# Kernel optimization log

Hardware: AMD Instinct MI355X
Metric: run time of the kernel (lower is better)

## Reference

```python
import jax, jax.numpy as jnp
import numpy as np

NUM_CLOTHES = 50000
FEAT_DIM = 256
BATCH = 1024
MOMENTUM = 0.0
SCALE = 16.0
EPSILON = 0.1


def setup_inputs() -> dict:
    key = jax.random.key(0)
    k1, k2, k3, k4 = jax.random.split(key, 4)
    inputs = jax.random.normal(k1, (BATCH, FEAT_DIM), dtype=jnp.float32)
    feature_memory = jax.random.normal(k2, (NUM_CLOTHES, FEAT_DIM), dtype=jnp.float32)
    targets = jax.random.randint(k3, (BATCH,), 0, NUM_CLOTHES, dtype=jnp.int64)
    # binary positive mask; guarantee the identity (own-clothes) column is positive
    positive_mask = (jax.random.uniform(k4, (BATCH, NUM_CLOTHES)) < 0.01).astype(jnp.float32)
    positive_mask = positive_mask.at[jnp.arange(BATCH), targets].set(1.0)
    return {"inputs": inputs, "feature_memory": feature_memory,
            "positive_mask": positive_mask, "targets": targets}


def _l2_normalize(x, axis=-1):
    # matches F.normalize(p=2): divide by max(||x||, 1e-12)
    n = jnp.sqrt(jnp.sum(x * x, axis=axis, keepdims=True))
    return x / jnp.maximum(n, 1e-12)


def reference(inputs, feature_memory, positive_mask, targets):
    B = inputs.shape[0]
    # ---- memory update: scatter-mean of detached features per clothes label ----
    feats = jax.lax.stop_gradient(inputs)
    sums = jax.ops.segment_sum(feats, targets, num_segments=NUM_CLOTHES)      # [C, D]
    counts = jax.ops.segment_sum(jnp.ones((B,), feats.dtype), targets,
                                 num_segments=NUM_CLOTHES)                     # [C]
    mean = sums / jnp.maximum(counts, 1.0)[:, None]
    present = (counts > 0)[:, None]
    memory = jnp.where(present,
                       MOMENTUM * feature_memory + (1.0 - MOMENTUM) * mean,
                       feature_memory)                                         # [C, D]
    memory = jax.lax.stop_gradient(memory)
    # ---- similarities against memory bank ----
    inputs_norm = _l2_normalize(inputs)
    memory_norm = _l2_normalize(memory)
    similarities = jnp.einsum('bd,cd->bc', inputs_norm, memory_norm) * SCALE   # [B, C]
    # ---- masked log-sum-exp loss ----
    negative_mask = 1.0 - positive_mask
    mask_identity = jax.nn.one_hot(targets, NUM_CLOTHES, dtype=similarities.dtype)
    exp_logits = jnp.exp(similarities)
    neg_sum = jnp.sum(exp_logits * negative_mask, axis=1, keepdims=True)       # [B, 1]
    log_prob = similarities - jnp.log(neg_sum + exp_logits)
    pos_count = jnp.sum(positive_mask, axis=1, keepdims=True)
    mask = (1.0 - EPSILON) * mask_identity + (EPSILON / pos_count) * positive_mask
    loss = jnp.mean(jnp.sum(-mask * log_prob, axis=1))
    return loss
```

## Files before the change

### kernel.cpp

```cpp
#include <hip/hip_runtime.h>
#include <hip/hip_bf16.h>
#include <stdint.h>

#define NCLOTHES 50000
#define CPAD     50048
#define NWORDS   782
#define NCB2     782
#define FDIM     256
#define NBATCH   1024
#define SCALEF   16.0f
#define EPSW     0.1f
#define SLOTS    8

typedef __attribute__((ext_vector_type(8))) short short8;
typedef __attribute__((ext_vector_type(4))) float f32x4;

__device__ __forceinline__ void gload_lds16(const void* gsrc, void* ldst) {
    __builtin_amdgcn_global_load_lds(
        (const __attribute__((address_space(1))) void*)gsrc,
        (__attribute__((address_space(3))) void*)ldst, 16, 0, 0);
}

__global__ __launch_bounds__(256)
void prep1_kernel(const float* __restrict__ in, const float* __restrict__ fm,
                  const float* __restrict__ pm,
                  __hip_bfloat16* __restrict__ A, __hip_bfloat16* __restrict__ Bm,
                  unsigned long long* __restrict__ maskw) {
    const int blk = blockIdx.x;
    const int t = threadIdx.x;

    if (blk < 1024) {
        int b = blk;
        float x = in[b * FDIM + t];
        float ss = x * x;
        #pragma unroll
        for (int o = 32; o > 0; o >>= 1) ss += __shfl_xor(ss, o);
        __shared__ float sh[4];
        if ((t & 63) == 0) sh[t >> 6] = ss;
        __syncthreads();
        float tot = sh[0] + sh[1] + sh[2] + sh[3];
        float r = SCALEF / fmaxf(sqrtf(tot), 1e-12f);
        A[b * FDIM + t] = __float2bfloat16(x * r);
    } else if (blk < 3072) {
        int p = blk - 1024;
        const int row = p >> 1;
        const int half = p & 1;
        const int wave = t >> 6;
        const int lane = t & 63;
        const float* prow = pm + (size_t)row * NCLOTHES;
        unsigned long long* wrow = maskw + (size_t)row * NWORDS;
        for (int chunk = half * 98 + wave; chunk < half * 98 + 98; chunk += 4) {
            int base = chunk * 256;
            int c0 = base + lane;
            float v0 = (c0 < NCLOTHES) ? prow[c0] : 0.f;
            float v1 = (c0 + 64 < NCLOTHES) ? prow[c0 + 64] : 0.f;
            float v2 = (c0 + 128 < NCLOTHES) ? prow[c0 + 128] : 0.f;
            float v3 = (c0 + 192 < NCLOTHES) ? prow[c0 + 192] : 0.f;
            unsigned long long b0 = __ballot(v0 >= 0.5f);
            unsigned long long b1 = __ballot(v1 >= 0.5f);
            unsigned long long b2 = __ballot(v2 >= 0.5f);
            unsigned long long b3 = __ballot(v3 >= 0.5f);
            if (lane < 4) {
                int wi = chunk * 4 + lane;
                unsigned long long w = (lane == 0) ? b0 : (lane == 1) ? b1 : (lane == 2) ? b2 : b3;
                if (wi < NWORDS) wrow[wi] = w;
            }
        }
    } else {
        const int nw = 2048 * 4;
        int w = ((blk - 3072) * 256 + t) >> 6;
        int lane = t & 63;
        for (int row = w; row < CPAD; row += nw) {
            __hip_bfloat16 h[4];
            if (row >= NCLOTHES) {
                h[0] = h[1] = h[2] = h[3] = __float2bfloat16(0.f);
            } else {
                f32x4 v = *(const f32x4*)(fm + (size_t)row * FDIM + lane * 4);
                float ss = v.x * v.x + v.y * v.y + v.z * v.z + v.w * v.w;
                #pragma unroll
                for (int o = 32; o > 0; o >>= 1) ss += __shfl_xor(ss, o);
                float r = 1.f / fmaxf(sqrtf(ss), 1e-12f);
                h[0] = __float2bfloat16(v.x * r);
                h[1] = __float2bfloat16(v.y * r);
                h[2] = __float2bfloat16(v.z * r);
                h[3] = __float2bfloat16(v.w * r);
            }
            *(ushort4*)(Bm + (size_t)row * FDIM + lane * 4) = *(const ushort4*)h;
        }
    }
}

__global__ void bnorm_present(const float* __restrict__ in, const int* __restrict__ tg,
                              __hip_bfloat16* __restrict__ Bm) {
    int b = blockIdx.x, t = threadIdx.x;
    __shared__ int stg[NBATCH];
    #pragma unroll
    for (int j = 0; j < 4; ++j) stg[t + j * 256] = tg[t + j * 256];
    __syncthreads();
    int c = stg[b];
    bool dup = false;
    #pragma unroll
    for (int j = 0; j < 4; ++j) {
        int i = t + j * 256;
        if (i < b && stg[i] == c) dup = true;
    }
    if (__syncthreads_or(dup)) return;
    __shared__ int mlist[64];
    __shared__ int mcount;
    if (t == 0) mcount = 0;
    __syncthreads();
    #pragma unroll
    for (int j = 0; j < 4; ++j) {
        int i = t + j * 256;
        if (stg[i] == c) { int p = atomicAdd(&mcount, 1); if (p < 64) mlist[p] = i; }
    }
    __syncthreads();
    int n = mcount;
    float v = 0.f;
    for (int i = 0; i < n; ++i) v += in[mlist[i] * FDIM + t];
    v /= (float)n;
    float ss = v * v;
    #pragma unroll
    for (int o = 32; o > 0; o >>= 1) ss += __shfl_xor(ss, o);
    __shared__ float sh[4];
    if ((t & 63) == 0) sh[t >> 6] = ss;
    __syncthreads();
    float tot = sh[0] + sh[1] + sh[2] + sh[3];
    float r = 1.0f / fmaxf(sqrtf(tot), 1e-12f);
    Bm[(size_t)c * FDIM + t] = __float2bfloat16(v * r);
}

#define BM 128
#define BN 128
#define BK 32
#define NKSTEP (FDIM / BK)

__global__ __launch_bounds__(256, 4)
void gemm_kernel(const __hip_bfloat16* __restrict__ A, const __hip_bfloat16* __restrict__ Bm,
                 const unsigned long long* __restrict__ maskw,
                 float* __restrict__ partial_ns,
                 float* __restrict__ sbuf)
{
    __shared__ alignas(16) __hip_bfloat16 As[2][BM * BK];
    __shared__ alignas(16) __hip_bfloat16 Bs[2][BM * BK];

    const int t = threadIdx.x;
    const int bx = blockIdx.x;
    const int bn0 = bx * BN;
    const int bm0 = blockIdx.y * BM;

    const int lane = t & 63;
    const int wave = t >> 6;
    const int wr = wave >> 1, wc = wave & 1;
    const int lrow = lane & 15, lq = lane >> 4;

    const int sr = t >> 2;
    const int sk = (t & 3) * 8;

    f32x4 acc[4][4];
    #pragma unroll
    for (int m = 0; m < 4; ++m)
        #pragma unroll
        for (int n = 0; n < 4; ++n) acc[m][n] = (f32x4)0.f;

    {
        const __hip_bfloat16* ag = A + (size_t)(bm0 + sr) * FDIM + sk;
        const __hip_bfloat16* bg = Bm + (size_t)(bn0 + sr) * FDIM + sk;
        gload_lds16(ag,             (void*)&As[0][t * 8]);
        gload_lds16(ag + 64 * FDIM, (void*)&As[0][2048 + t * 8]);
        gload_lds16(bg,             (void*)&Bs[0][t * 8]);
        gload_lds16(bg + 64 * FDIM, (void*)&Bs[0][2048 + t * 8]);
    }

    for (int ks = 0; ks < NKSTEP; ++ks) {
        __syncthreads();
        int cur = ks & 1;
        if (ks + 1 < NKSTEP) {
            int nxt = cur ^ 1;
            int k0 = (ks + 1) * BK;
            const __hip_bfloat16* ag = A + (size_t)(bm0 + sr) * FDIM + k0 + sk;
            const __hip_bfloat16* bg = Bm + (size_t)(bn0 + sr) * FDIM + k0 + sk;
            gload_lds16(ag,             (void*)&As[nxt][t * 8]);
            gload_lds16(ag + 64 * FDIM, (void*)&As[nxt][2048 + t * 8]);
            gload_lds16(bg,             (void*)&Bs[nxt][t * 8]);
            gload_lds16(bg + 64 * FDIM, (void*)&Bs[nxt][2048 + t * 8]);
        }
        short8 af[4], bf[4];
        #pragma unroll
        for (int m = 0; m < 4; ++m)
            af[m] = *(const short8*)&As[cur][(wr * 64 + m * 16 + lrow) * BK + lq * 8];
        #pragma unroll
        for (int n = 0; n < 4; ++n)
            bf[n] = *(const short8*)&Bs[cur][(wc * 64 + n * 16 + lrow) * BK + lq * 8];
        #pragma unroll
        for (int m = 0; m < 4; ++m)
            #pragma unroll
            for (int n = 0; n < 4; ++n)
                acc[m][n] = __builtin_amdgcn_mfma_f32_16x16x32_bf16(af[m], bf[n], acc[m][n], 0, 0, 0);
    }

    const int rowbase = bm0 + wr * 64;
    const int colbase = bn0 + wc * 64;
    const int cb2 = bx * 2 + wc;

    #pragma unroll
    for (int m = 0; m < 4; ++m) {
        #pragma unroll
        for (int r = 0; r < 4; ++r) {
            const int grow = rowbase + m * 16 + lq * 4 + r;
            const unsigned long long mw = maskw[(size_t)grow * NWORDS + cb2];
            float pneg = 0.f;
            #pragma unroll
            for (int n = 0; n < 4; ++n) {
                const int p = n * 16 + lrow;
                bool vld = (colbase + p) < NCLOTHES;
                bool pos = (mw >> p) & 1ull;
                pneg += (vld && !pos) ? __expf(acc[m][n][r]) : 0.f;
            }
            pneg += __shfl_xor(pneg, 1);
            pneg += __shfl_xor(pneg, 2);
            pneg += __shfl_xor(pneg, 4);
            pneg += __shfl_xor(pneg, 8);
            const size_t srow = (size_t)grow * NCB2 + cb2;
            #pragma unroll
            for (int n = 0; n < 4; ++n) {
                const int p = n * 16 + lrow;
                if ((mw >> p) & 1ull) {
                    int pre = __popcll(mw & ((1ull << p) - 1ull));
                    if (pre < SLOTS) sbuf[srow * SLOTS + pre] = acc[m][n][r];
                }
            }
            if (lrow == 0) partial_ns[(size_t)cb2 * NBATCH + grow] = pneg;
        }
    }
}

__global__ void nsum_kernel(const float* __restrict__ partial_ns, float* __restrict__ negsum) {
    int b = blockIdx.x * 256 + threadIdx.x;
    float s = 0.f;
    #pragma unroll 8
    for (int cb = 0; cb < NCB2; ++cb) s += partial_ns[(size_t)cb * NBATCH + b];
    negsum[b] = s;
}

__global__ void finish_kernel(const float* __restrict__ negsum,
                              const unsigned long long* __restrict__ maskw,
                              const float* __restrict__ sbuf,
                              const int* __restrict__ tg, float* __restrict__ loss_rows) {
    int b = blockIdx.x, t = threadIdx.x;
    int tgt = tg[b];
    const int cbt = tgt >> 6, bitp = tgt & 63;
    const float ns = negsum[b];

    const unsigned long long* mrow = maskw + (size_t)b * NWORDS;
    const float* srow = sbuf + (size_t)b * NCB2 * SLOTS;

    float slp = 0.f, idlp = 0.f;
    int np = 0;
    for (int cb = t; cb < NCB2; cb += 256) {
        unsigned long long mw = mrow[cb];
        if (mw) {
            int k = __popcll(mw);
            np += k;
            int kk = k < SLOTS ? k : SLOTS;
            const float* sp = srow + (size_t)cb * SLOTS;
            for (int i = 0; i < kk; ++i) {
                float s = sp[i];
                slp += s - __logf(ns + __expf(s));
            }
            if (cb == cbt) {
                int idslot = __popcll(mw & ((1ull << bitp) - 1ull));
                if (idslot < SLOTS) {
                    float s = sp[idslot];
                    idlp = s - __logf(ns + __expf(s));
                }
            }
        }
    }
    #pragma unroll
    for (int o = 32; o > 0; o >>= 1) {
        slp += __shfl_xor(slp, o);
        idlp += __shfl_xor(idlp, o);
        np += __shfl_xor(np, o);
    }
    __shared__ float sh1[4], sh2[4];
    __shared__ int shp[4];
    if ((t & 63) == 0) { sh1[t >> 6] = slp; sh2[t >> 6] = idlp; shp[t >> 6] = np; }
    __syncthreads();
    if (t == 0) {
        float s_all = sh1[0] + sh1[1] + sh1[2] + sh1[3];
        float i_all = sh2[0] + sh2[1] + sh2[2] + sh2[3];
        int np_all = shp[0] + shp[1] + shp[2] + shp[3];
        loss_rows[b] = -((1.0f - EPSW) * i_all + (EPSW / (float)np_all) * s_all);
    }
}

__global__ void reduce_kernel(const float* __restrict__ lr, float* __restrict__ out) {
    int t = threadIdx.x;
    float s = lr[t] + lr[t + 256] + lr[t + 512] + lr[t + 768];
    #pragma unroll
    for (int o = 32; o > 0; o >>= 1) s += __shfl_xor(s, o);
    __shared__ float sh[4];
    if ((t & 63) == 0) sh[t >> 6] = s;
    __syncthreads();
    if (t == 0) out[0] = (sh[0] + sh[1] + sh[2] + sh[3]) * (1.0f / NBATCH);
}

extern "C" void kernel_launch(void* const* d_in, const int* in_sizes, int n_in,
                              void* d_out, int out_size, void* d_ws, size_t ws_size,
                              hipStream_t stream) {
    const float* inputs  = (const float*)d_in[0];
    const float* fm      = (const float*)d_in[1];
    const float* pmask   = (const float*)d_in[2];
    const int*   targets = (const int*)d_in[3];
    float* out = (float*)d_out;

    char* ws = (char*)d_ws;
    size_t off = 0;
    __hip_bfloat16* A = (__hip_bfloat16*)(ws + off);  off += (size_t)NBATCH * FDIM * 2;
    __hip_bfloat16* Bm = (__hip_bfloat16*)(ws + off); off += (size_t)CPAD * FDIM * 2;
    off = (off + 255) & ~(size_t)255;
    unsigned long long* maskw = (unsigned long long*)(ws + off); off += (size_t)NBATCH * NWORDS * 8;
    float* partial_ns = (float*)(ws + off);        off += (size_t)NCB2 * NBATCH * 4;
    float* sbuf = (float*)(ws + off);              off += (size_t)NBATCH * NCB2 * SLOTS * 4;
    float* negsum = (float*)(ws + off);            off += 4096;
    float* loss_rows = (float*)(ws + off);         off += 4096;

    prep1_kernel<<<5120, 256, 0, stream>>>(inputs, fm, pmask, A, Bm, maskw);
    bnorm_present<<<NBATCH, 256, 0, stream>>>(inputs, targets, Bm);
    gemm_kernel<<<dim3(CPAD / BN, NBATCH / BM), 256, 0, stream>>>(A, Bm, maskw, partial_ns, sbuf);
    nsum_kernel<<<4, 256, 0, stream>>>(partial_ns, negsum);
    finish_kernel<<<NBATCH, 256, 0, stream>>>(negsum, maskw, sbuf, targets, loss_rows);
    reduce_kernel<<<1, 256, 0, stream>>>(loss_rows, out);
}
```

Before: 502.6 us.

## Keep 64-column memory tile resident in LDS and stream batch rows through

The GEMM now gives each block a 64-column slice of the normalized memory bank. That slice is loaded into LDS once, with XOR swizzling, and the block loops over all 1024 batch rows in 128-row chunks, double-buffering only the A tiles. Each memory-bank row is read from global memory once instead of once per batch tile, at the cost of a larger LDS footprint and lower occupancy (launch bounds drop from 4 to 3). The fused prep kernel is split into three separate kernels, and the negative-sum reduction is split across 8 column chunks combined with atomics. The atomic combine makes the float summation order nondeterministic.

```diff
diff --git a/kernel.cpp b/kernel.cpp
--- a/kernel.cpp
+++ b/kernel.cpp
@@ -21,72 +21,70 @@
         (__attribute__((address_space(3))) void*)ldst, 16, 0, 0);
 }
 
+__global__ void anorm_kernel(const float* __restrict__ in, __hip_bfloat16* __restrict__ A,
+                             float* __restrict__ negsum) {
+    int b = blockIdx.x, t = threadIdx.x;
+    if (t == 0) negsum[b] = 0.f;
+    float x = in[b * FDIM + t];
+    float ss = x * x;
+    #pragma unroll
+    for (int o = 32; o > 0; o >>= 1) ss += __shfl_xor(ss, o);
+    __shared__ float sh[4];
+    if ((t & 63) == 0) sh[t >> 6] = ss;
+    __syncthreads();
+    float tot = sh[0] + sh[1] + sh[2] + sh[3];
+    float r = SCALEF / fmaxf(sqrtf(tot), 1e-12f);
+    A[b * FDIM + t] = __float2bfloat16(x * r);
+}
+
 __global__ __launch_bounds__(256)
-void prep1_kernel(const float* __restrict__ in, const float* __restrict__ fm,
-                  const float* __restrict__ pm,
-                  __hip_bfloat16* __restrict__ A, __hip_bfloat16* __restrict__ Bm,
-                  unsigned long long* __restrict__ maskw) {
-    const int blk = blockIdx.x;
-    const int t = threadIdx.x;
-
-    if (blk < 1024) {
-        int b = blk;
-        float x = in[b * FDIM + t];
-        float ss = x * x;
-        #pragma unroll
-        for (int o = 32; o > 0; o >>= 1) ss += __shfl_xor(ss, o);
-        __shared__ float sh[4];
-        if ((t & 63) == 0) sh[t >> 6] = ss;
-        __syncthreads();
-        float tot = sh[0] + sh[1] + sh[2] + sh[3];
-        float r = SCALEF / fmaxf(sqrtf(tot), 1e-12f);
-        A[b * FDIM + t] = __float2bfloat16(x * r);
-    } else if (blk < 3072) {
-        int p = blk - 1024;
-        const int row = p >> 1;
-        const int half = p & 1;
-        const int wave = t >> 6;
-        const int lane = t & 63;
-        const float* prow = pm + (size_t)row * NCLOTHES;
-        unsigned long long* wrow = maskw + (size_t)row * NWORDS;
-        for (int chunk = half * 98 + wave; chunk < half * 98 + 98; chunk += 4) {
-            int base = chunk * 256;
-            int c0 = base + lane;
-            float v0 = (c0 < NCLOTHES) ? prow[c0] : 0.f;
-            float v1 = (c0 + 64 < NCLOTHES) ? prow[c0 + 64] : 0.f;
-            float v2 = (c0 + 128 < NCLOTHES) ? prow[c0 + 128] : 0.f;
-            float v3 = (c0 + 192 < NCLOTHES) ? prow[c0 + 192] : 0.f;
-            unsigned long long b0 = __ballot(v0 >= 0.5f);
-            unsigned long long b1 = __ballot(v1 >= 0.5f);
-            unsigned long long b2 = __ballot(v2 >= 0.5f);
-            unsigned long long b3 = __ballot(v3 >= 0.5f);
-            if (lane < 4) {
-                int wi = chunk * 4 + lane;
-                unsigned long long w = (lane == 0) ? b0 : (lane == 1) ? b1 : (lane == 2) ? b2 : b3;
-                if (wi < NWORDS) wrow[wi] = w;
-            }
-        }
-    } else {
-        const int nw = 2048 * 4;
-        int w = ((blk - 3072) * 256 + t) >> 6;
-        int lane = t & 63;
-        for (int row = w; row < CPAD; row += nw) {
-            __hip_bfloat16 h[4];
-            if (row >= NCLOTHES) {
-                h[0] = h[1] = h[2] = h[3] = __float2bfloat16(0.f);
-            } else {
-                f32x4 v = *(const f32x4*)(fm + (size_t)row * FDIM + lane * 4);
-                float ss = v.x * v.x + v.y * v.y + v.z * v.z + v.w * v.w;
-                #pragma unroll
-                for (int o = 32; o > 0; o >>= 1) ss += __shfl_xor(ss, o);
-                float r = 1.f / fmaxf(sqrtf(ss), 1e-12f);
-                h[0] = __float2bfloat16(v.x * r);
-                h[1] = __float2bfloat16(v.y * r);
-                h[2] = __float2bfloat16(v.z * r);
-                h[3] = __float2bfloat16(v.w * r);
-            }
-            *(ushort4*)(Bm + (size_t)row * FDIM + lane * 4) = *(const ushort4*)h;
-        }
+void pack_kernel(const float* __restrict__ pm, unsigned long long* __restrict__ maskw) {
+    const int row = blockIdx.x;
+    const int half = blockIdx.y;
+    const int wave = threadIdx.x >> 6;
+    const int lane = threadIdx.x & 63;
+    const float* prow = pm + (size_t)row * NCLOTHES;
+    unsigned long long* wrow = maskw + (size_t)row * NWORDS;
+    for (int chunk = half * 98 + wave; chunk < half * 98 + 98; chunk += 4) {
+        int base = chunk * 256;
+        int c0 = base + lane;
+        float v0 = (c0 < NCLOTHES) ? prow[c0] : 0.f;
+        float v1 = (c0 + 64 < NCLOTHES) ? prow[c0 + 64] : 0.f;
+        float v2 = (c0 + 128 < NCLOTHES) ? prow[c0 + 128] : 0.f;
+        float v3 = (c0 + 192 < NCLOTHES) ? prow[c0 + 192] : 0.f;
+        unsigned long long b0 = __ballot(v0 >= 0.5f);
+        unsigned long long b1 = __ballot(v1 >= 0.5f);
+        unsigned long long b2 = __ballot(v2 >= 0.5f);
+        unsigned long long b3 = __ballot(v3 >= 0.5f);
+        if (lane < 4) {
+            int wi = chunk * 4 + lane;
+            unsigned long long w = (lane == 0) ? b0 : (lane == 1) ? b1 : (lane == 2) ? b2 : b3;
+            if (wi < NWORDS) wrow[wi] = w;
+        }
+    }
+}
+
+__global__ __launch_bounds__(256)
+void bnorm_all(const float* __restrict__ fm, __hip_bfloat16* __restrict__ Bm) {
+    const int nw = (gridDim.x * 256) >> 6;
+    int w = (blockIdx.x * 256 + threadIdx.x) >> 6;
+    int lane = threadIdx.x & 63;
+    for (int row = w; row < CPAD; row += nw) {
+        __hip_bfloat16 h[4];
+        if (row >= NCLOTHES) {
+            h[0] = h[1] = h[2] = h[3] = __float2bfloat16(0.f);
+        } else {
+            f32x4 v = *(const f32x4*)(fm + (size_t)row * FDIM + lane * 4);
+            float ss = v.x * v.x + v.y * v.y + v.z * v.z + v.w * v.w;
+            #pragma unroll
+            for (int o = 32; o > 0; o >>= 1) ss += __shfl_xor(ss, o);
+            float r = 1.f / fmaxf(sqrtf(ss), 1e-12f);
+            h[0] = __float2bfloat16(v.x * r);
+            h[1] = __float2bfloat16(v.y * r);
+            h[2] = __float2bfloat16(v.z * r);
+            h[3] = __float2bfloat16(v.w * r);
+        }
+        *(ushort4*)(Bm + (size_t)row * FDIM + lane * 4) = *(const ushort4*)h;
     }
 }
 
@@ -130,117 +128,120 @@
     Bm[(size_t)c * FDIM + t] = __float2bfloat16(v * r);
 }
 
-#define BM 128
-#define BN 128
-#define BK 32
-#define NKSTEP (FDIM / BK)
-
-__global__ __launch_bounds__(256, 4)
+__global__ __launch_bounds__(256, 3)
 void gemm_kernel(const __hip_bfloat16* __restrict__ A, const __hip_bfloat16* __restrict__ Bm,
                  const unsigned long long* __restrict__ maskw,
                  float* __restrict__ partial_ns,
                  float* __restrict__ sbuf)
 {
-    __shared__ alignas(16) __hip_bfloat16 As[2][BM * BK];
-    __shared__ alignas(16) __hip_bfloat16 Bs[2][BM * BK];
+    __shared__ alignas(16) __hip_bfloat16 Bs[64 * FDIM];
+    __shared__ alignas(16) __hip_bfloat16 As[2][128 * 32];
 
     const int t = threadIdx.x;
     const int bx = blockIdx.x;
-    const int bn0 = bx * BN;
-    const int bm0 = blockIdx.y * BM;
+    const int colbase = bx * 64;
 
     const int lane = t & 63;
-    const int wave = t >> 6;
-    const int wr = wave >> 1, wc = wave & 1;
+    const int w = t >> 6;
     const int lrow = lane & 15, lq = lane >> 4;
 
-    const int sr = t >> 2;
-    const int sk = (t & 3) * 8;
-
-    f32x4 acc[4][4];
-    #pragma unroll
-    for (int m = 0; m < 4; ++m)
+    {
+        const int brow = colbase + (t >> 5);
+        const int bel = (((t & 31) ^ (t >> 5)) << 3);
+        const __hip_bfloat16* bsrc = Bm + (size_t)brow * FDIM + bel;
+        #pragma unroll
+        for (int j = 0; j < 8; ++j)
+            gload_lds16(bsrc + (size_t)j * 8 * FDIM, (void*)&Bs[j * 2048 + t * 8]);
+    }
+    const int arow_t = t >> 2;
+    const int ael_t = (((t & 3) ^ ((t >> 2) & 3)) << 3);
+    {
+        const __hip_bfloat16* asrc = A + (size_t)arow_t * FDIM + ael_t;
+        gload_lds16(asrc,                       (void*)&As[0][t * 8]);
+        gload_lds16(asrc + (size_t)64 * FDIM,   (void*)&As[0][2048 + t * 8]);
+    }
+
+    f32x4 acc[2][4];
+    #pragma unroll
+    for (int m = 0; m < 2; ++m)
         #pragma unroll
         for (int n = 0; n < 4; ++n) acc[m][n] = (f32x4)0.f;
 
-    {
-        const __hip_bfloat16* ag = A + (size_t)(bm0 + sr) * FDIM + sk;
-        const __hip_bfloat16* bg = Bm + (size_t)(bn0 + sr) * FDIM + sk;
-        gload_lds16(ag,             (void*)&As[0][t * 8]);
-        gload_lds16(ag + 64 * FDIM, (void*)&As[0][2048 + t * 8]);
-        gload_lds16(bg,             (void*)&Bs[0][t * 8]);
-        gload_lds16(bg + 64 * FDIM, (void*)&Bs[0][2048 + t * 8]);
-    }
-
-    for (int ks = 0; ks < NKSTEP; ++ks) {
-        __syncthreads();
-        int cur = ks & 1;
-        if (ks + 1 < NKSTEP) {
-            int nxt = cur ^ 1;
-            int k0 = (ks + 1) * BK;
-            const __hip_bfloat16* ag = A + (size_t)(bm0 + sr) * FDIM + k0 + sk;
-            const __hip_bfloat16* bg = Bm + (size_t)(bn0 + sr) * FDIM + k0 + sk;
-            gload_lds16(ag,             (void*)&As[nxt][t * 8]);
-            gload_lds16(ag + 64 * FDIM, (void*)&As[nxt][2048 + t * 8]);
-            gload_lds16(bg,             (void*)&Bs[nxt][t * 8]);
-            gload_lds16(bg + 64 * FDIM, (void*)&Bs[nxt][2048 + t * 8]);
-        }
-        short8 af[4], bf[4];
-        #pragma unroll
-        for (int m = 0; m < 4; ++m)
-            af[m] = *(const short8*)&As[cur][(wr * 64 + m * 16 + lrow) * BK + lq * 8];
-        #pragma unroll
-        for (int n = 0; n < 4; ++n)
-            bf[n] = *(const short8*)&Bs[cur][(wc * 64 + n * 16 + lrow) * BK + lq * 8];
-        #pragma unroll
-        for (int m = 0; m < 4; ++m)
-            #pragma unroll
-            for (int n = 0; n < 4; ++n)
-                acc[m][n] = __builtin_amdgcn_mfma_f32_16x16x32_bf16(af[m], bf[n], acc[m][n], 0, 0, 0);
-    }
-
-    const int rowbase = bm0 + wr * 64;
-    const int colbase = bn0 + wc * 64;
-    const int cb2 = bx * 2 + wc;
-
-    #pragma unroll
-    for (int m = 0; m < 4; ++m) {
-        #pragma unroll
-        for (int r = 0; r < 4; ++r) {
-            const int grow = rowbase + m * 16 + lq * 4 + r;
-            const unsigned long long mw = maskw[(size_t)grow * NWORDS + cb2];
-            float pneg = 0.f;
+    for (int bd = 0; bd < 8; ++bd) {
+        #pragma unroll
+        for (int ks = 0; ks < 8; ++ks) {
+            const int step = bd * 8 + ks;
+            const int cur = step & 1;
+            __syncthreads();
+            if (step + 1 < 64) {
+                const int ns = step + 1;
+                const __hip_bfloat16* asrc = A + (size_t)((ns >> 3) * 128 + arow_t) * FDIM
+                                               + (ns & 7) * 32 + ael_t;
+                gload_lds16(asrc,                     (void*)&As[cur ^ 1][t * 8]);
+                gload_lds16(asrc + (size_t)64 * FDIM, (void*)&As[cur ^ 1][2048 + t * 8]);
+            }
+            short8 af[2], bf[4];
+            #pragma unroll
+            for (int m = 0; m < 2; ++m) {
+                int row = w * 32 + m * 16 + lrow;
+                af[m] = *(const short8*)&As[cur][row * 32 + ((lq ^ (row & 3)) << 3)];
+            }
             #pragma unroll
             for (int n = 0; n < 4; ++n) {
-                const int p = n * 16 + lrow;
-                bool vld = (colbase + p) < NCLOTHES;
-                bool pos = (mw >> p) & 1ull;
-                pneg += (vld && !pos) ? __expf(acc[m][n][r]) : 0.f;
-            }
-            pneg += __shfl_xor(pneg, 1);
-            pneg += __shfl_xor(pneg, 2);
-            pneg += __shfl_xor(pneg, 4);
-            pneg += __shfl_xor(pneg, 8);
-            const size_t srow = (size_t)grow * NCB2 + cb2;
-            #pragma unroll
-            for (int n = 0; n < 4; ++n) {
-                const int p = n * 16 + lrow;
-                if ((mw >> p) & 1ull) {
-                    int pre = __popcll(mw & ((1ull << p) - 1ull));
-                    if (pre < SLOTS) sbuf[srow * SLOTS + pre] = acc[m][n][r];
+                int cr = n * 16 + lrow;
+                bf[n] = *(const short8*)&Bs[cr * 256 + (((ks * 4 + lq) ^ (cr & 7)) << 3)];
+            }
+            #pragma unroll
+            for (int m = 0; m < 2; ++m)
+                #pragma unroll
+                for (int n = 0; n < 4; ++n)
+                    acc[m][n] = __builtin_amdgcn_mfma_f32_16x16x32_bf16(af[m], bf[n], acc[m][n], 0, 0, 0);
+        }
+
+        #pragma unroll
+        for (int m = 0; m < 2; ++m) {
+            #pragma unroll
+            for (int rr = 0; rr < 4; ++rr) {
+                const int grow = bd * 128 + w * 32 + m * 16 + lq * 4 + rr;
+                const unsigned long long mw = maskw[(size_t)grow * NWORDS + bx];
+                float pneg = 0.f;
+                #pragma unroll
+                for (int n = 0; n < 4; ++n) {
+                    const int p = n * 16 + lrow;
+                    bool vld = (colbase + p) < NCLOTHES;
+                    bool pos = (mw >> p) & 1ull;
+                    pneg += (vld && !pos) ? __expf(acc[m][n][rr]) : 0.f;
                 }
-            }
-            if (lrow == 0) partial_ns[(size_t)cb2 * NBATCH + grow] = pneg;
-        }
+                pneg += __shfl_xor(pneg, 1);
+                pneg += __shfl_xor(pneg, 2);
+                pneg += __shfl_xor(pneg, 4);
+                pneg += __shfl_xor(pneg, 8);
+                const size_t srow = (size_t)grow * NCB2 + bx;
+                #pragma unroll
+                for (int n = 0; n < 4; ++n) {
+                    const int p = n * 16 + lrow;
+                    if ((mw >> p) & 1ull) {
+                        int pre = __popcll(mw & ((1ull << p) - 1ull));
+                        if (pre < SLOTS) sbuf[srow * SLOTS + pre] = acc[m][n][rr];
+                    }
+                }
+                if (lrow == 0) partial_ns[(size_t)bx * NBATCH + grow] = pneg;
+            }
+        }
+        #pragma unroll
+        for (int m = 0; m < 2; ++m)
+            #pragma unroll
+            for (int n = 0; n < 4; ++n) acc[m][n] = (f32x4)0.f;
     }
 }
 
 __global__ void nsum_kernel(const float* __restrict__ partial_ns, float* __restrict__ negsum) {
     int b = blockIdx.x * 256 + threadIdx.x;
+    int cb0 = blockIdx.y * 98;
+    int cb1 = cb0 + 98; if (cb1 > NWORDS) cb1 = NWORDS;
     float s = 0.f;
-    #pragma unroll 8
-    for (int cb = 0; cb < NCB2; ++cb) s += partial_ns[(size_t)cb * NBATCH + b];
-    negsum[b] = s;
+    for (int cb = cb0; cb < cb1; ++cb) s += partial_ns[(size_t)cb * NBATCH + b];
+    atomicAdd(&negsum[b], s);
 }
 
 __global__ void finish_kernel(const float* __restrict__ negsum,
@@ -321,15 +322,17 @@
     __hip_bfloat16* Bm = (__hip_bfloat16*)(ws + off); off += (size_t)CPAD * FDIM * 2;
     off = (off + 255) & ~(size_t)255;
     unsigned long long* maskw = (unsigned long long*)(ws + off); off += (size_t)NBATCH * NWORDS * 8;
-    float* partial_ns = (float*)(ws + off);        off += (size_t)NCB2 * NBATCH * 4;
+    float* partial_ns = (float*)(ws + off);        off += (size_t)NWORDS * NBATCH * 4;
     float* sbuf = (float*)(ws + off);              off += (size_t)NBATCH * NCB2 * SLOTS * 4;
     float* negsum = (float*)(ws + off);            off += 4096;
     float* loss_rows = (float*)(ws + off);         off += 4096;
 
-    prep1_kernel<<<5120, 256, 0, stream>>>(inputs, fm, pmask, A, Bm, maskw);
+    anorm_kernel<<<NBATCH, 256, 0, stream>>>(inputs, A, negsum);
+    pack_kernel<<<dim3(NBATCH, 2), 256, 0, stream>>>(pmask, maskw);
+    bnorm_all<<<2048, 256, 0, stream>>>(fm, Bm);
     bnorm_present<<<NBATCH, 256, 0, stream>>>(inputs, targets, Bm);
-    gemm_kernel<<<dim3(CPAD / BN, NBATCH / BM), 256, 0, stream>>>(A, Bm, maskw, partial_ns, sbuf);
-    nsum_kernel<<<4, 256, 0, stream>>>(partial_ns, negsum);
+    gemm_kernel<<<NWORDS, 256, 0, stream>>>(A, Bm, maskw, partial_ns, sbuf);
+    nsum_kernel<<<dim3(4, 8), 256, 0, stream>>>(partial_ns, negsum);
     finish_kernel<<<NBATCH, 256, 0, stream>>>(negsum, maskw, sbuf, targets, loss_rows);
     reduce_kernel<<<1, 256, 0, stream>>>(loss_rows, out);
 }
```

Result: slower. 523.0 us (+4.0%).
